# Kernel tuning notes

Measured on AMD Instinct MI355X. Metric: run time of the kernel, lower is better.

Reference implementation:

```python
import jax, jax.numpy as jnp
import numpy as np
import math

B, C_IN, C_OUT, H, W = 16, 128, 128, 56, 56
K, S, P, D = 3, 1, 1, 1
PROD_KS = K * K


def _unfold(x, k, s, p, d):
    # torch.nn.functional.unfold equivalent -> (B, k*k, C, Ho*Wo)
    b, c, h, w = x.shape
    ho = (h + 2 * p - d * (k - 1) - 1) // s + 1
    wo = (w + 2 * p - d * (k - 1) - 1) // s + 1
    xp = jnp.pad(x, ((0, 0), (0, 0), (p, p), (p, p)))
    patches = [
        xp[:, :, i * d: i * d + (ho - 1) * s + 1: s, j * d: j * d + (wo - 1) * s + 1: s]
        for i in range(k) for j in range(k)
    ]
    u = jnp.stack(patches, axis=1)  # (B, K2, C, Ho, Wo)
    return u.reshape(b, k * k, c, ho * wo), ho, wo


def setup_inputs() -> dict:
    key = jax.random.key(0)
    k1, k2, k3, k4 = jax.random.split(key, 4)
    stdv = 1.0 / math.sqrt(C_IN * PROD_KS)
    x = jax.random.normal(k1, (B, C_IN, H, W), dtype=jnp.float32)
    weight = jax.random.uniform(k2, (1, PROD_KS, C_OUT, C_IN), dtype=jnp.float32,
                                minval=-stdv, maxval=stdv)
    b_k = jax.random.uniform(k3, (1, PROD_KS, 1, C_OUT, 1), dtype=jnp.float32,
                             minval=-stdv, maxval=stdv)
    bias = jax.random.uniform(k4, (C_OUT,), dtype=jnp.float32, minval=-stdv, maxval=stdv)
    return {"x": x, "weight": weight, "b_k": b_k, "bias": bias}


def reference(x, weight, b_k, bias):
    batch = x.shape[0]
    u, ho, wo = _unfold(x, K, S, P, D)          # (B, K2, C_in, L)
    inpt = u.transpose(0, 1, 3, 2)               # (B, K2, L, C_in)
    # GEMM: (B,K2,L,Cin) x (K2,Cout,Cin) -> (B,K2,L,Cout)
    out = jnp.einsum('bklc,koc->bklo', inpt, weight[0])
    bk = b_k[0, :, 0, :, 0]                      # (K2, Cout)
    # fused cos/sin contraction over kernel positions -> (B, L, Cout) each
    a = jnp.einsum('bklo,ko->blo', out, jnp.cos(bk))
    bb = jnp.einsum('bklo,ko->blo', out, jnp.sin(bk))
    eps = 1e-05
    a_gt = a > 0
    b_gt = bb > 0
    ab_eq = a_gt == b_gt
    theta = jnp.where(ab_eq, jnp.arctan(bb / (a + eps)), -jnp.arctan(a / (bb + eps)))
    pi = math.pi
    peak = jnp.where(ab_eq & a_gt, pi / 2.0,
           jnp.where(ab_eq & ~a_gt, -pi / 2.0,
           jnp.where(~ab_eq & ~b_gt, -pi, 0.0)))
    theta = peak - theta
    o = jnp.sin(theta) * a + jnp.cos(theta) * bb  # (B, L, Cout)
    o = o.transpose(0, 2, 1) + bias[None, :, None]  # (B, Cout, L)
    conv_out = o.reshape(batch, C_OUT, ho, wo)
    theta_out = (theta / pi).transpose(0, 2, 1).reshape(batch, C_OUT, ho, wo)
    return jnp.concatenate([conv_out, theta_out], axis=1)
```

## Files before the change

### kernel.cpp

```cpp
#include <hip/hip_runtime.h>
#include <hip/hip_bf16.h>
#include <math.h>

#define NB   16
#define CIN  128
#define COUT 128
#define HH   56
#define WW   56
#define LL   3136

typedef __attribute__((ext_vector_type(8))) short short8;
typedef __attribute__((ext_vector_type(16))) float f32x16;
typedef __attribute__((ext_vector_type(4))) float f32x4;
typedef __attribute__((ext_vector_type(4))) unsigned int uint4v;

#define PXT    256
#define NPXT   13
#define XC     58
#define XPLANE 7424
#define XUSH   14848
#define XUNITS 1856
#define XHALF  928
#define CPW    16
#define WS_TAP 1024
#define WS_N   9216
#define WUSH   18432
#define WBYTES 36864
#define WUNITS 2304

#define XT_ROWS 62
#define XT_PLANE_USH (XT_ROWS*XC*16)
#define XT_CG_STRIDE 3682304

#define CSD_OFF 256
#define WSP_OFF 32768
#define XT_OFF  1212416
#define XT_SIZE 29458432
#define WL_OFF  (XT_OFF + XT_SIZE)

__global__ void prep_kernel(const float* __restrict__ w, const float* __restrict__ bk,
                            const float* __restrict__ x,
                            double* __restrict__ csd, unsigned short* __restrict__ wsp,
                            unsigned short* __restrict__ xt, unsigned* __restrict__ cnt) {
    int bid = blockIdx.x;
    if (bid == 0 && threadIdx.x == 0) *cnt = 0u;
    if (bid < 576) {
        int i = bid * 256 + threadIdx.x;
        if (i >= 9*COUT*CIN) return;
        int k = i / (COUT*CIN);
        int rem = i - k*(COUT*CIN);
        int oc = rem >> 7, c = rem & 127;
        double bkv = (double)bk[k*COUT + oc];
        double ck = cos(bkv), sk = sin(bkv);
        if (c == 0) {
            csd[k*COUT + oc]          = ck;
            csd[9*COUT + k*COUT + oc] = sk;
        }
        float wv = w[i];
        float fa = (float)(ck * (double)wv);
        float fb = (float)(sk * (double)wv);
        __hip_bfloat16 ah = __float2bfloat16(fa);
        __hip_bfloat16 al = __float2bfloat16(fa - __bfloat162float(ah));
        __hip_bfloat16 bh = __float2bfloat16(fb);
        __hip_bfloat16 bl = __float2bfloat16(fb - __bfloat162float(bh));
        int ocb = oc >> 5;
        int rowa = oc & 31, rowb = 32 + rowa;
        int cg = c >> 4, cp = c & 15;
        int sl = (((cp >> 3) ^ ((rowa >> 2) & 1)) << 3) | (cp & 7);
        size_t img = ((size_t)ocb*8 + cg) * (WBYTES/2);
        wsp[img + (size_t)k*WS_TAP + rowa*CPW + sl]        = *(unsigned short*)&ah;
        wsp[img + (size_t)k*WS_TAP + rowb*CPW + sl]        = *(unsigned short*)&bh;
        wsp[img + WS_N + (size_t)k*WS_TAP + rowa*CPW + sl] = *(unsigned short*)&al;
        wsp[img + WS_N + (size_t)k*WS_TAP + rowb*CPW + sl] = *(unsigned short*)&bl;
    } else {
        int i = (bid - 576) * 256 + threadIdx.x;
        if (i < 100352) {
            int c4 = i % 14; int t = i / 14;
            int row1 = t % 56; t /= 56;
            int bat = t & 15, cg = t >> 4;
            const float* xp = x + ((size_t)(bat*CIN + cg*16))*LL + row1*WW + c4*4;
            unsigned short hi[4][16], lo[4][16];
            #pragma unroll
            for (int j = 0; j < 16; j++) {
                f32x4 v = *(const f32x4*)(xp + (size_t)j*LL);
                #pragma unroll
                for (int cc = 0; cc < 4; cc++) {
                    float f = v[cc];
                    __hip_bfloat16 h = __float2bfloat16(f);
                    __hip_bfloat16 l = __float2bfloat16(f - __bfloat162float(h));
                    hi[cc][j] = *(unsigned short*)&h;
                    lo[cc][j] = *(unsigned short*)&l;
                }
            }
            size_t base = ((((size_t)cg*16 + bat)*2 + 0)*XT_ROWS + (row1+1))*XC + (c4*4 + 1);
            #pragma unroll
            for (int cc = 0; cc < 4; cc++) {
                unsigned short* dh = xt + (base + cc)*16;
                unsigned short* dl = dh + XT_PLANE_USH;
                *(uint4v*)dh       = *(const uint4v*)&hi[cc][0];
                *(uint4v*)(dh + 8) = *(const uint4v*)&hi[cc][8];
                *(uint4v*)dl       = *(const uint4v*)&lo[cc][0];
                *(uint4v*)(dl + 8) = *(const uint4v*)&lo[cc][8];
            }
        } else if (i < 218112) {
            int i2 = i - 100352;
            int unit = i2 % 460; int t = i2 / 460;
            int pl = t & 1; t >>= 1;
            int bat = t & 15, cg = t >> 4;
            int row, c58;
            if (unit < 348) {
                int zr = unit / 58; c58 = unit - zr*58;
                row = (zr == 0) ? 0 : (56 + zr);
            } else {
                int u2 = unit - 348; row = 1 + (u2 >> 1); c58 = (u2 & 1) ? 57 : 0;
            }
            size_t base = ((((size_t)cg*16 + bat)*2 + pl)*XT_ROWS + row)*XC + c58;
            uint4v zz = {0u,0u,0u,0u};
            *(uint4v*)(xt + base*16)     = zz;
            *(uint4v*)(xt + base*16 + 8) = zz;
        }
    }
}

__global__ __launch_bounds__(512, 4)
void mfma_kernel(const unsigned short* __restrict__ xt, const unsigned short* __restrict__ wsp,
                 const float* __restrict__ bias, float* __restrict__ out,
                 unsigned* __restrict__ cnt, unsigned* __restrict__ wl, unsigned cap)
{
    __shared__ __align__(16) unsigned short SM[XUSH + WUSH];
    __shared__ float sm_bias[32];

    const int tid = threadIdx.x;
    int bid = blockIdx.x;
    int wk = (bid & 7) * 104 + (bid >> 3);
    const int ocb = wk & 3; wk >>= 2;
    const int pxt = wk % NPXT;
    const int bat = wk / NPXT;
    const int l0  = pxt * PXT;
    const int o0  = ocb * 32;
    const int yf  = l0 / WW;

    const int lane = tid & 63;
    const int n    = lane & 31;
    const int kh   = lane >> 5;
    const int wave = tid >> 6;

    if (tid < 32) sm_bias[tid] = bias[o0 + tid];

    unsigned xoff[4];
    #pragma unroll
    for (int k = 0; k < 4; k++) {
        int u = tid + 512*k;
        int uc = u < XUNITS ? u : XUNITS-1;
        int pl = uc >= XHALF ? 1 : 0;
        int rem = uc - pl*XHALF;
        int q  = rem >> 1;
        int hl = rem & 1;
        int hg = hl ^ ((q >> 2) & 1);
        int r  = q / XC;
        int c  = q - r*XC;
        xoff[k] = (unsigned)((((bat*2 + pl)*XT_ROWS + (yf + r))*XC + c)*32 + hg*16);
    }

    int p  = l0 + wave*32 + n;
    int pc = p < LL ? p : LL-1;
    int py = pc / WW, pxx = pc - py*WW;
    const int q0 = (py - yf)*XC + pxx;

    const int sw  = ((((n>>2)&1) ^ kh) << 3);
    const int iAa = n*CPW + sw;
    const int iAb = (32+n)*CPW + sw;

    f32x16 acc_a, acc_b;
    #pragma unroll
    for (int r = 0; r < 16; r++) { acc_a[r] = 0.f; acc_b[r] = 0.f; }

    const char* xtB  = (const char*)xt;
    const char* wspB = (const char*)wsp + (size_t)ocb * (8*(size_t)WBYTES);

    auto stage_x = [&](int chn) {
        const char* xp = xtB + (size_t)chn * XT_CG_STRIDE;
        #pragma unroll
        for (int k = 0; k < 3; k++) {
            __builtin_amdgcn_global_load_lds(
                (const __attribute__((address_space(1))) unsigned int*)(xp + xoff[k]),
                (__attribute__((address_space(3))) unsigned int*)&SM[(wave*64 + 512*k)*8],
                16, 0, 0);
        }
        if (wave < 5)
            __builtin_amdgcn_global_load_lds(
                (const __attribute__((address_space(1))) unsigned int*)(xp + xoff[3]),
                (__attribute__((address_space(3))) unsigned int*)&SM[(1536 + wave*64)*8],
                16, 0, 0);
    };
    auto stage_w = [&](int chn) {
        const char* wp = wspB + (size_t)chn * (size_t)WBYTES;
        #pragma unroll
        for (int k = 0; k < 4; k++) {
            __builtin_amdgcn_global_lo\
ad_lds(
                (const __attribute__((address_space(1))) unsigned int*)(wp + (tid + 512*k)*16),
                (__attribute__((address_space(3))) unsigned int*)&SM[XUSH + (wave*64 + 512*k)*8],
                16, 0, 0);
        }
        if (wave < 4)
            __builtin_amdgcn_global_load_lds(
                (const __attribute__((address_space(1))) unsigned int*)(wp + (2048 + tid)*16),
                (__attribute__((address_space(3))) unsigned int*)&SM[XUSH + (2048 + wave*64)*8],
                16, 0, 0);
    };

    stage_x(0);
    stage_w(0);
    __syncthreads();

    #pragma unroll 1
    for (int ch = 0; ch < 8; ch++) {
        #pragma unroll
        for (int tap = 0; tap < 9; tap++) {
            const int ky = tap / 3, kx = tap - 3*ky;
            short8 Aha = *(const short8*)&SM[XUSH + tap*WS_TAP + iAa];
            short8 Ahb = *(const short8*)&SM[XUSH + tap*WS_TAP + iAb];
            short8 Ala = *(const short8*)&SM[XUSH + WS_N + tap*WS_TAP + iAa];
            short8 Alb = *(const short8*)&SM[XUSH + WS_N + tap*WS_TAP + iAb];
            int q  = q0 + ky*XC + kx;
            int si = q*16 + ((kh ^ ((q>>2)&1)) << 3);
            short8 Bh = *(const short8*)&SM[si];
            short8 Bl = *(const short8*)&SM[XPLANE + si];
            __builtin_amdgcn_s_setprio(1);
            acc_a = __builtin_amdgcn_mfma_f32_32x32x16_bf16(Ala, Bh, acc_a, 0,0,0);
            acc_a = __builtin_amdgcn_mfma_f32_32x32x16_bf16(Aha, Bl, acc_a, 0,0,0);
            acc_a = __builtin_amdgcn_mfma_f32_32x32x16_bf16(Aha, Bh, acc_a, 0,0,0);
            acc_b = __builtin_amdgcn_mfma_f32_32x32x16_bf16(Alb, Bh, acc_b, 0,0,0);
            acc_b = __builtin_amdgcn_mfma_f32_32x32x16_bf16(Ahb, Bl, acc_b, 0,0,0);
            acc_b = __builtin_amdgcn_mfma_f32_32x32x16_bf16(Ahb, Bh, acc_b, 0,0,0);
            __builtin_amdgcn_s_setprio(0);
        }
        if (ch < 7) {
            __syncthreads();
            stage_x(ch+1);
            stage_w(ch+1);
            __syncthreads();
        }
    }

    const float eps = 1e-05f;
    const float PIf = 3.14159265358979323846f;
    size_t obase = (size_t)bat * (2*COUT) * LL;
    const int pcol = wave*32 + n;
    const int pp = l0 + pcol;

    #pragma unroll
    for (int r = 0; r < 16; r++) {
        int row = (r & 3) + 8*(r >> 2) + 4*kh;
        float av = acc_a[r];
        float bv = acc_b[r];
        bool flag = (pp < LL) &&
                    (fabsf(av) < 1.5e-4f || (bv < 1.05e-5f && bv > -2.05e-5f));
        unsigned long long m = __ballot(flag);
        if (m) {
            int leader = (int)__ffsll((long long)m) - 1;
            unsigned base = 0;
            if (lane == leader) base = atomicAdd(cnt, (unsigned)__popcll(m));
            base = __shfl(base, leader);
            if (flag) {
                unsigned slot = base + (unsigned)__popcll(m & ((1ULL << lane) - 1ULL));
                if (slot < cap)
                    wl[slot] = ((unsigned)(bat*LL + pp) << 7) | (unsigned)(o0 + row);
            }
        }
        bool ag = av > 0.f, bg = bv > 0.f;
        bool eq = (ag == bg);
        float ratio = eq ? (bv / (av + eps)) : (av / (bv + eps));
        float at = atanf(ratio);
        float peak = eq ? (ag ? PIf*0.5f : -PIf*0.5f) : (bg ? 0.0f : -PIf);
        float th = peak - (eq ? at : -at);
        float c = 1.0f / sqrtf(1.0f + ratio*ratio);
        float t = eq ? (av + ratio*bv) : (ratio*av + bv);
        bool pos = eq ? ag : bg;
        float o = (pos ? c : -c) * t;
        if (pp < LL) {
            out[obase + (size_t)(o0+row)*LL + pp]      = o + sm_bias[row];
            out[obase + (size_t)(COUT+o0+row)*LL + pp] = th * (1.0f/PIf);
        }
    }
}

__global__ __launch_bounds__(256)
void fixup_kernel(const float* __restrict__ x, const float* __restrict__ w,
                  const double* __restrict__ csd, const float* __restrict__ bias,
                  const unsigned* __restrict__ cnt, const unsigned* __restrict__ wl,
                  unsigned cap, float* __restrict__ out) {
    const int lane   = threadIdx.x & 63;
    const int waveid = (blockIdx.x * 256 + threadIdx.x) >> 6;
    const int nwaves = gridDim.x * 4;
    unsigned nf = *cnt; if (nf > cap) nf = cap;
    const double PI = 3.14159265358979323846;

    for (unsigned u = waveid; u < nf; u += nwaves) {
        unsigned idx = wl[u];
        int oc = idx & 127;
        unsigned rest = idx >> 7;
        int bb_ = rest / LL;
        int l   = rest - bb_*LL;
        int yy  = l / WW;
        int xx  = l - yy*WW;
        const float* xb = x + (size_t)bb_ * CIN * LL;

        double pa = 0.0, pb = 0.0;
        #pragma unroll
        for (int k = 0; k < 9; k++) {
            int dy = k/3, dx = k - dy*3;
            int py = yy + dy - 1, px = xx + dx - 1;
            double pk = 0.0;
            if ((unsigned)py < HH && (unsigned)px < WW) {
                int base = py*WW + px;
                const float* wr = w + k*(COUT*CIN) + oc*CIN;
                int c = lane;
                pk  = (double)xb[(size_t)c*LL + base] * (double)wr[c];
                c = lane + 64;
                pk += (double)xb[(size_t)c*LL + base] * (double)wr[c];
            }
            pa += csd[k*COUT + oc] * pk;
            pb += csd[9*COUT + k*COUT + oc] * pk;
        }
        #pragma unroll
        for (int off = 32; off > 0; off >>= 1) {
            pa += __shfl_xor(pa, off, 64);
            pb += __shfl_xor(pb, off, 64);
        }
        if (lane == 0) {
            bool ag = pa > 0.0, bg = pb > 0.0;
            bool eq = (ag == bg);
            double th;
            if (eq) th = (ag ? PI*0.5 : -PI*0.5) - atan(pb / (pa + 1e-5));
            else    th = (bg ? 0.0 : -PI) + atan(pa / (pb + 1e-5));
            double o = sin(th)*pa + cos(th)*pb + (double)bias[oc];
            out[((size_t)bb_*(2*COUT) + oc) * LL + l]        = (float)o;
            out[((size_t)bb_*(2*COUT) + COUT + oc) * LL + l] = (float)(th / PI);
        }
    }
}

extern "C" void kernel_launch(void* const* d_in, const int* in_sizes, int n_in,
                              void* d_out, int out_size, void* d_ws, size_t ws_size,
                              hipStream_t stream) {
    const float* x    = (const float*)d_in[0];
    const float* w    = (const float*)d_in[1];
    const float* bk   = (const float*)d_in[2];
    const float* bias = (const float*)d_in[3];
    float* out = (float*)d_out;

    char* ws = (char*)d_ws;
    unsigned*       cnt = (unsigned*)ws;
    double*         csd = (double*)(ws + CSD_OFF);
    unsigned short* wsp = (unsigned short*)(ws + WSP_OFF);
    unsigned short* xt  = (unsigned short*)(ws + XT_OFF);
    unsigned*       wl  = (unsigned*)(ws + WL_OFF);
    unsigned cap = (ws_size > (size_t)WL_OFF + 4096) ? (unsigned)((ws_size - WL_OFF) / 4) : 0u;

    hipLaunchKernelGGL(prep_kernel,  dim3(1428), dim3(256), 0, stream,
                       w, bk, x, csd, wsp, xt, cnt);
    hipLaunchKernelGGL(mfma_kernel,  dim3(NB*NPXT*4), dim3(512), 0, stream,
                       xt, wsp, bias, out, cnt, wl, cap);
    hipLaunchKernelGGL(fixup_kernel, dim3(256), dim3(256), 0, stream,
                       x, w, csd, bias, cnt, wl, cap, out);
}
```

Baseline: 330.9 us.

## Double-buffer LDS staging of activations and weights across channel chunks

Splits shared memory into two ping-pong buffers each for activation and weight tiles. The next channel chunk is prefetched with global_load_lds before computing on the current one, so one barrier per chunk replaces two and the load latency can overlap with MFMA work. This doubles LDS use per block to about 132 KB, which cuts resident blocks per CU, so the launch bounds are relaxed to 1 block.

New measurement: 338.5 us. 1.02x slower.

```diff
diff --git a/kernel.cpp b/kernel.cpp
--- a/kernel.cpp
+++ b/kernel.cpp
@@ -26,7 +26,6 @@
 #define WS_N   9216
 #define WUSH   18432
 #define WBYTES 36864
-#define WUNITS 2304
 
 #define XT_ROWS 62
 #define XT_PLANE_USH (XT_ROWS*XC*16)
@@ -122,12 +121,13 @@
     }
 }
 
-__global__ __launch_bounds__(512, 4)
+__global__ __launch_bounds__(512, 1)
 void mfma_kernel(const unsigned short* __restrict__ xt, const unsigned short* __restrict__ wsp,
                  const float* __restrict__ bias, float* __restrict__ out,
                  unsigned* __restrict__ cnt, unsigned* __restrict__ wl, unsigned cap)
 {
-    __shared__ __align__(16) unsigned short SM[XUSH + WUSH];
+    __shared__ __align__(16) unsigned short SMX[2*XUSH];
+    __shared__ __align__(16) unsigned short SMW[2*WUSH];
     __shared__ float sm_bias[32];
 
     const int tid = threadIdx.x;
@@ -180,33 +180,34 @@
 
     auto stage_x = [&](int chn) {
         const char* xp = xtB + (size_t)chn * XT_CG_STRIDE;
+        unsigned short* dst = &SMX[(chn & 1) * XUSH];
         #pragma unroll
         for (int k = 0; k < 3; k++) {
             __builtin_amdgcn_global_load_lds(
                 (const __attribute__((address_space(1))) unsigned int*)(xp + xoff[k]),
-                (__attribute__((address_space(3))) unsigned int*)&SM[(wave*64 + 512*k)*8],
+                (__attribute__((address_space(3))) unsigned int*)&dst[(wave*64 + 512*k)*8],
                 16, 0, 0);
         }
         if (wave < 5)
             __builtin_amdgcn_global_load_lds(
                 (const __attribute__((address_space(1))) unsigned int*)(xp + xoff[3]),
-                (__attribute__((address_space(3))) unsigned int*)&SM[(1536 + wave*64)*8],
+                (__attribute__((address_space(3))) unsigned int*)&dst[(1536 + wave*64)*8],
                 16, 0, 0);
     };
     auto stage_w = [&](int chn) {
         const char* wp = wspB + (size_t)chn * (size_t)WBYTES;
+        unsigned short* dst = &SMW[(chn & 1) * WUSH];
         #pragma unroll
         for (int k = 0; k < 4; k++) {
-            __builtin_amdgcn_global_lo\
-ad_lds(
+            __builtin_amdgcn_global_load_lds(
                 (const __attribute__((address_space(1))) unsigned int*)(wp + (tid + 512*k)*16),
-                (__attribute__((address_space(3))) unsigned int*)&SM[XUSH + (wave*64 + 512*k)*8],
+                (__attribute__((address_space(3))) unsigned int*)&dst[(wave*64 + 512*k)*8],
                 16, 0, 0);
         }
         if (wave < 4)
             __builtin_amdgcn_global_load_lds(
                 (const __attribute__((address_space(1))) unsigned int*)(wp + (2048 + tid)*16),
-                (__attribute__((address_space(3))) unsigned int*)&SM[XUSH + (2048 + wave*64)*8],
+                (__attribute__((address_space(3))) unsigned int*)&dst[(2048 + wave*64)*8],
                 16, 0, 0);
     };
 
@@ -216,17 +217,20 @@
 
     #pragma unroll 1
     for (int ch = 0; ch < 8; ch++) {
+        if (ch < 7) { stage_x(ch+1); stage_w(ch+1); }
+        const unsigned short* smx = &SMX[(ch & 1) * XUSH];
+        const unsigned short* smw = &SMW[(ch & 1) * WUSH];
         #pragma unroll
         for (int tap = 0; tap < 9; tap++) {
             const int ky = tap / 3, kx = tap - 3*ky;
-            short8 Aha = *(const short8*)&SM[XUSH + tap*WS_TAP + iAa];
-            short8 Ahb = *(const short8*)&SM[XUSH + tap*WS_TAP + iAb];
-            short8 Ala = *(const short8*)&SM[XUSH + WS_N + tap*WS_TAP + iAa];
-            short8 Alb = *(const short8*)&SM[XUSH + WS_N + tap*WS_TAP + iAb];
+            short8 Aha = *(const short8*)&smw[tap*WS_TAP + iAa];
+            short8 Ahb = *(const short8*)&smw[tap*WS_TAP + iAb];
+            short8 Ala = *(const short8*)&smw[WS_N + tap*WS_TAP + iAa];
+            short8 Alb = *(const short8*)&smw[WS_N + tap*WS_TAP + iAb];
             int q  = q0 + ky*XC + kx;
             int si = q*16 + ((kh ^ ((q>>2)&1)) << 3);
-            short8 Bh = *(const short8*)&SM[si];
-            short8 Bl = *(const short8*)&SM[XPLANE + si];
+            short8 Bh = *(const short8*)&smx[si];
+            short8 Bl = *(const short8*)&smx[XPLANE + si];
             __builtin_amdgcn_s_setprio(1);
             acc_a = __builtin_amdgcn_mfma_f32_32x32x16_bf16(Ala, Bh, acc_a, 0,0,0);
             acc_a = __builtin_amdgcn_mfma_f32_32x32x16_bf16(Aha, Bl, acc_a, 0,0,0);
@@ -236,12 +240,7 @@
             acc_b = __builtin_amdgcn_mfma_f32_32x32x16_bf16(Ahb, Bh, acc_b, 0,0,0);
             __builtin_amdgcn_s_setprio(0);
         }
-        if (ch < 7) {
-            __syncthreads();
-            stage_x(ch+1);
-            stage_w(ch+1);
-            __syncthreads();
-        }
+        if (ch < 7) __syncthreads();
     }
 
     const float eps = 1e-05f;
```

## Halve workgroup size so each wave computes two pixel groups, reusing weight fragments

Applied to the files above, without the earlier changes.

The MFMA kernel drops from 512 to 256 threads per block, and each wave now handles two 32-pixel groups. The A (weight) fragments loaded from LDS are reused across both groups, which halves LDS weight reads per MFMA. The weight image is re-laid out in prep so each lane reads a contiguous 16-byte chunk per tap and part, and the XOR swizzle is removed. Weight prep also switches from double to float cos/sin products, which saves prep time at a small precision risk. Accumulator registers double, so occupancy may drop (launch bounds now 256,2).

New measurement: 338.4 us. 1.02x slower.

```diff
diff --git a/kernel.cpp b/kernel.cpp
--- a/kernel.cpp
+++ b/kernel.cpp
@@ -21,12 +21,10 @@
 #define XUSH   14848
 #define XUNITS 1856
 #define XHALF  928
-#define CPW    16
-#define WS_TAP 1024
-#define WS_N   9216
 #define WUSH   18432
 #define WBYTES 36864
 #define WUNITS 2304
+
 
 #define XT_ROWS 62
 #define XT_PLANE_USH (XT_ROWS*XC*16)
@@ -50,28 +48,30 @@
         int k = i / (COUT*CIN);
         int rem = i - k*(COUT*CIN);
         int oc = rem >> 7, c = rem & 127;
-        double bkv = (double)bk[k*COUT + oc];
-        double ck = cos(bkv), sk = sin(bkv);
+        float bkv = bk[k*COUT + oc];
         if (c == 0) {
-            csd[k*COUT + oc]          = ck;
-            csd[9*COUT + k*COUT + oc] = sk;
-        }
+            double bd = (double)bkv;
+            csd[k*COUT + oc]          = cos(bd);
+            csd[9*COUT + k*COUT + oc] = sin(bd);
+        }
+        float ck = cosf(bkv), sk = sinf(bkv);
         float wv = w[i];
-        float fa = (float)(ck * (double)wv);
-        float fb = (float)(sk * (double)wv);
+        float fa = ck * wv;
+        float fb = sk * wv;
         __hip_bfloat16 ah = __float2bfloat16(fa);
         __hip_bfloat16 al = __float2bfloat16(fa - __bfloat162float(ah));
         __hip_bfloat16 bh = __float2bfloat16(fb);
         __hip_bfloat16 bl = __float2bfloat16(fb - __bfloat162float(bh));
         int ocb = oc >> 5;
-        int rowa = oc & 31, rowb = 32 + rowa;
+        int rowa = oc & 31;
         int cg = c >> 4, cp = c & 15;
-        int sl = (((cp >> 3) ^ ((rowa >> 2) & 1)) << 3) | (cp & 7);
-        size_t img = ((size_t)ocb*8 + cg) * (WBYTES/2);
-        wsp[img + (size_t)k*WS_TAP + rowa*CPW + sl]        = *(unsigned short*)&ah;
-        wsp[img + (size_t)k*WS_TAP + rowb*CPW + sl]        = *(unsigned short*)&bh;
-        wsp[img + WS_N + (size_t)k*WS_TAP + rowa*CPW + sl] = *(unsigned short*)&al;
-        wsp[img + WS_N + (size_t)k*WS_TAP + rowb*CPW + sl] = *(unsigned short*)&bl;
+        int lane = rowa + ((cp >> 3) << 5);
+        int bp = cp & 7;
+        size_t img = ((size_t)ocb*8 + cg) * WUSH;
+        wsp[img + (size_t)((k*4+0)*64 + lane)*8 + bp] = *(unsigned short*)&ah;
+        wsp[img + (size_t)((k*4+1)*64 + lane)*8 + bp] = *(unsigned short*)&bh;
+        wsp[img + (size_t)((k*4+2)*64 + lane)*8 + bp] = *(unsigned short*)&al;
+        wsp[img + (size_t)((k*4+3)*64 + lane)*8 + bp] = *(unsigned short*)&bl;
     } else {
         int i = (bid - 576) * 256 + threadIdx.x;
         if (i < 100352) {
@@ -122,12 +122,13 @@
     }
 }
 
-__global__ __launch_bounds__(512, 4)
+__global__ __launch_bounds__(256, 2)
 void mfma_kernel(const unsigned short* __restrict__ xt, const unsigned short* __restrict__ wsp,
                  const float* __restrict__ bias, float* __restrict__ out,
                  unsigned* __restrict__ cnt, unsigned* __restrict__ wl, unsigned cap)
 {
-    __shared__ __align__(16) unsigned short SM[XUSH + WUSH];
+    __shared__ __align__(16) unsigned short SMX[XUSH];
+    __shared__ __align__(16) unsigned short SMW[WUSH];
     __shared__ float sm_bias[32];
 
     const int tid = threadIdx.x;
@@ -147,10 +148,10 @@
 
     if (tid < 32) sm_bias[tid] = bias[o0 + tid];
 
-    unsigned xoff[4];
+    unsigned xoff[8];
     #pragma unroll
-    for (int k = 0; k < 4; k++) {
-        int u = tid + 512*k;
+    for (int k = 0; k < 8; k++) {
+        int u = tid + 256*k;
         int uc = u < XUNITS ? u : XUNITS-1;
         int pl = uc >= XHALF ? 1 : 0;
         int rem = uc - pl*XHALF;
@@ -162,18 +163,21 @@
         xoff[k] = (unsigned)((((bat*2 + pl)*XT_ROWS + (yf + r))*XC + c)*32 + hg*16);
     }
 
-    int p  = l0 + wave*32 + n;
-    int pc = p < LL ? p : LL-1;
-    int py = pc / WW, pxx = pc - py*WW;
-    const int q0 = (py - yf)*XC + pxx;
-
-    const int sw  = ((((n>>2)&1) ^ kh) << 3);
-    const int iAa = n*CPW + sw;
-    const int iAb = (32+n)*CPW + sw;
-
-    f32x16 acc_a, acc_b;
+    int q0g[2];
     #pragma unroll
-    for (int r = 0; r < 16; r++) { acc_a[r] = 0.f; acc_b[r] = 0.f; }
+    for (int g = 0; g < 2; g++) {
+        int p  = l0 + wave*64 + g*32 + n;
+        int pc = p < LL ? p : LL-1;
+        int py = pc / WW, pxx = pc - py*WW;
+        q0g[g] = (py - yf)*XC + pxx;
+    }
+
+    f32x16 acc_a[2], acc_b[2];
+    #pragma unroll
+    for (int g = 0; g < 2; g++) {
+        #pragma unroll
+        for (int r = 0; r < 16; r++) { acc_a[g][r] = 0.f; acc_b[g][r] = 0.f; }
+    }
 
     const char* xtB  = (const char*)xt;
     const char* wspB = (const char*)wsp + (size_t)ocb * (8*(size_t)WBYTES);
@@ -181,59 +185,58 @@
     auto stage_x = [&](int chn) {
         const char* xp = xtB + (size_t)chn * XT_CG_STRIDE;
         #pragma unroll
-        for (int k = 0; k < 3; k++) {
+        for (int k = 0; k < 7; k++) {
             __builtin_amdgcn_global_load_lds(
                 (const __attribute__((address_space(1))) unsigned int*)(xp + xoff[k]),
-                (__attribute__((address_space(3))) unsigned int*)&SM[(wave*64 + 512*k)*8],
+                (__attribute__((address_space(3))) unsigned int*)&SMX[(wave*64 + 256*k)*8],
                 16, 0, 0);
         }
-        if (wave < 5)
+        if (wave == 0)
             __builtin_amdgcn_global_load_lds(
-                (const __attribute__((address_space(1))) unsigned int*)(xp + xoff[3]),
-                (__attribute__((address_space(3))) unsigned int*)&SM[(1536 + wave*64)*8],
+                (const __attribute__((address_space(1))) unsigned int*)(xp + xoff[7]),
+                (__attribute__((address_space(3))) unsigned int*)&SMX[1792*8],
                 16, 0, 0);
     };
     auto stage_w = [&](int chn) {
         const char* wp = wspB + (size_t)chn * (size_t)WBYTES;
         #pragma unroll
-        for (int k = 0; k < 4; k++) {
-            __builtin_amdgcn_global_lo\
-ad_lds(
-                (const __attribute__((address_space(1))) unsigned int*)(wp + (tid + 512*k)*16),
-                (__attribute__((address_space(3))) unsigned int*)&SM[XUSH + (wave*64 + 512*k)*8],
+        for (int k = 0; k < 9; k++) {
+            __builtin_amdgcn_global_load_lds(
+                (const __attribute__((address_space(1))) unsigned int*)(wp + (tid + 256*k)*16),
+                (__attribute__((address_space(3))) unsigned int*)&SMW[(wave*64 + 256*k)*8],
                 16, 0, 0);
         }
-        if (wave < 4)
-            __builtin_amdgcn_global_load_lds(
-                (const __attribute__((address_space(1))) unsigned int*)(wp + (2048 + tid)*16),
-                (__attribute__((address_space(3))) unsigned int*)&SM[XUSH + (2048 + wave*64)*8],
-                16, 0, 0);
     };
 
     stage_x(0);
     stage_w(0);
     __syncthreads();
 
+    const unsigned short* awp = &SMW[lane*8];
+
     #pragma unroll 1
     for (int ch = 0; ch < 8; ch++) {
         #pragma unroll
         for (int tap = 0; tap < 9; tap++) {
             const int ky = tap / 3, kx = tap - 3*ky;
-            short8 Aha = *(const short8*)&SM[XUSH + tap*WS_TAP + iAa];
-            short8 Ahb = *(const short8*)&SM[XUSH + tap*WS_TAP + iAb];
-            short8 Ala = *(const short8*)&SM[XUSH + WS_N + tap*WS_TAP + iAa];
-            short8 Alb = *(const short8*)&SM[XUSH + WS_N + tap*WS_TAP + iAb];
-            int q  = q0 + ky*XC + kx;
-            int si = q*16 + ((kh ^ ((q>>2)&1)) << 3);
-            short8 Bh = *(const short8*)&SM[si];
-            short8 Bl = *(const short8*)&SM[XPLANE + si];
+            short8 Aha = *(const short8*)&awp[(tap*4+0)*512];
+            short8 Ahb = *(const short8*)&awp[(tap*4+1)*512];
+            short8 Ala = *(const short8*)&awp[(tap*4+2)*512];
+            short8 Alb = *(const short8*)&awp[(tap*4+3)*512];
             __builtin_amdgcn_s_setprio(1);
-            acc_a = __builtin_amdgcn_mfma_f32_32x32x16_bf16(Ala, Bh, acc_a, 0,0,0);
-            acc_a = __builtin_amdgcn_mfma_f32_32x32x16_bf16(Aha, Bl, acc_a, 0,0,0);
-            acc_a = __builtin_amdgcn_mfma_f32_32x32x16_bf16(Aha, Bh, acc_a, 0,0,0);
-            acc_b = __builtin_amdgcn_mfma_f32_32x32x16_bf16(Alb, Bh, acc_b, 0,0,0);
-            acc_b = __builtin_amdgcn_mfma_f32_32x32x16_bf16(Ahb, Bl, acc_b, 0,0,0);
-            acc_b = __builtin_amdgcn_mfma_f32_32x32x16_bf16(Ahb, Bh, acc_b, 0,0,0);
+            #pragma unroll
+            for (int g = 0; g < 2; g++) {
+                int q  = q0g[g] + ky*XC + kx;
+                int si = q*16 + ((kh ^ ((q>>2)&1)) << 3);
+                short8 Bh = *(const short8*)&SMX[si];
+                short8 Bl = *(const short8*)&SMX[XPLANE + si];
+                acc_a[g] = __builtin_amdgcn_mfma_f32_32x32x16_bf16(Ala, Bh, acc_a[g], 0,0,0);
+                acc_a[g] = __builtin_amdgcn_mfma_f32_32x32x16_bf16(Aha, Bl, acc_a[g], 0,0,0);
+                acc_a[g] = __builtin_amdgcn_mfma_f32_32x32x16_bf16(Aha, Bh, acc_a[g], 0,0,0);
+                acc_b[g] = __builtin_amdgcn_mfma_f32_32x32x16_bf16(Alb, Bh, acc_b[g], 0,0,0);
+                acc_b[g] = __builtin_amdgcn_mfma_f32_32x32x16_bf16(Ahb, Bl, acc_b[g], 0,0,0);
+                acc_b[g] = __builtin_amdgcn_mfma_f32_32x32x16_bf16(Ahb, Bh, acc_b[g], 0,0,0);
+            }
             __builtin_amdgcn_s_setprio(0);
         }
         if (ch < 7) {
@@ -247,41 +250,44 @@
     const float eps = 1e-05f;
     const float PIf = 3.14159265358979323846f;
     size_t obase = (size_t)bat * (2*COUT) * LL;
-    const int pcol = wave*32 + n;
-    const int pp = l0 + pcol;
 
     #pragma unroll
-    for (int r = 0; r < 16; r++) {
-        int row = (r & 3) + 8*(r >> 2) + 4*kh;
-        float av = acc_a[r];
-        float bv = acc_b[r];
-        bool flag = (pp < LL) &&
-                    (fabsf(av) < 1.5e-4f || (bv < 1.05e-5f && bv > -2.05e-5f));
-        unsigned long long m = __ballot(flag);
-        if (m) {
-            int leader = (int)__ffsll((long long)m) - 1;
-            unsigned base = 0;
-            if (lane == leader) base = atomicAdd(cnt, (unsigned)__popcll(m));
-            base = __shfl(base, leader);
-            if (flag) {
-                unsigned slot = base + (unsigned)__popcll(m & ((1ULL << lane) - 1ULL));
-                if (slot < cap)
-                    wl[slot] = ((unsigned)(bat*LL + pp) << 7) | (unsigned)(o0 + row);
-            }
-        }
-        bool ag = av > 0.f, bg = bv > 0.f;
-        bool eq = (ag == bg);
-        float ratio = eq ? (bv / (av + eps)) : (av / (bv + eps));
-        float at = atanf(ratio);
-        float peak = eq ? (ag ? PIf*0.5f : -PIf*0.5f) : (bg ? 0.0f : -PIf);
-        float th = peak - (eq ? at : -at);
-        float c = 1.0f / sqrtf(1.0f + ratio*ratio);
-        float t = eq ? (av + ratio*bv) : (ratio*av + bv);
-        bool pos = eq ? ag : bg;
-        float o = (pos ? c : -c) * t;
-        if (pp < LL) {
-            out[obase + (size_t)(o0+row)*LL + pp]      = o + sm_bias[row];
-            out[obase + (size_t)(COUT+o0+row)*LL + pp] = th * (1.0f/PIf);
+    for (int g = 0; g < 2; g++) {
+        const int pcol = wave*64 + g*32 + n;
+        const int pp = l0 + pcol;
+        #pragma unroll
+        for (int r = 0; r < 16; r++) {
+            int row = (r & 3) + 8*(r >> 2) + 4*kh;
+            float av = acc_a[g][r];
+            float bv = acc_b[g][r];
+            bool flag = (pp < LL) &&
+                        (fabsf(av) < 1.5e-4f || (bv < 1.05e-5f && bv > -2.05e-5f));
+            unsigned long long m = __ballot(flag);
+            if (m) {
+                int leader = (int)__ffsll((long long)m) - 1;
+                unsigned base = 0;
+                if (lane == leader) base = atomicAdd(cnt, (unsigned)__popcll(m));
+                base = __shfl(base, leader);
+                if (flag) {
+                    unsigned slot = base + (unsigned)__popcll(m & ((1ULL << lane) - 1ULL));
+                    if (slot < cap)
+                        wl[slot] = ((unsigned)(bat*LL + pp) << 7) | (unsigned)(o0 + row);
+                }
+            }
+            bool ag = av > 0.f, bg = bv > 0.f;
+            bool eq = (ag == bg);
+            float ratio = eq ? (bv / (av + eps)) : (av / (bv + eps));
+            float at = atanf(ratio);
+            float peak = eq ? (ag ? PIf*0.5f : -PIf*0.5f) : (bg ? 0.0f : -PIf);
+            float th = peak - (eq ? at : -at);
+            float c = 1.0f / sqrtf(1.0f + ratio*ratio);
+            float t = eq ? (av + ratio*bv) : (ratio*av + bv);
+            bool pos = eq ? ag : bg;
+            float o = (pos ? c : -c) * t;
+            if (pp < LL) {
+                out[obase + (size_t)(o0+row)*LL + pp]      = o + sm_bias[row];
+                out[obase + (size_t)(COUT+o0+row)*LL + pp] = th * (1.0f/PIf);
+            }
         }
     }
 }
@@ -361,7 +367,7 @@
 
     hipLaunchKernelGGL(prep_kernel,  dim3(1428), dim3(256), 0, stream,
                        w, bk, x, csd, wsp, xt, cnt);
-    hipLaunchKernelGGL(mfma_kernel,  dim3(NB*NPXT*4), dim3(512), 0, stream,
+    hipLaunchKernelGGL(mfma_kernel,  dim3(NB*NPXT*4), dim3(256), 0, stream,
                        xt, wsp, bias, out, cnt, wl, cap);
     hipLaunchKernelGGL(fixup_kernel, dim3(256), dim3(256), 0, stream,
                        x, w, csd, bias, cnt, wl, cap, out);
```
